# Performance work log

Measured on AMD Instinct MI355X. Metric: run time of the kernel, lower is better.

The kernel has to match this reference:

```python
import jax, jax.numpy as jnp
import numpy as np
import math

N_HEAD = 16
HEAD_DIM = 64  # n_embd // n_head = 1024 / 16
N_EMBD = 1024
B, T = 4, 4096
LIN_K = 1024


def setup_inputs() -> dict:
    key = jax.random.key(0)
    ks = jax.random.split(key, 7)
    s = 0.02
    return {
        "x": jax.random.normal(ks[0], (B, T, N_EMBD), dtype=jnp.float32),
        "W_attn": jax.random.normal(ks[1], (N_EMBD, 3 * N_EMBD), dtype=jnp.float32) * s,
        "b_attn": jax.random.normal(ks[2], (3 * N_EMBD,), dtype=jnp.float32) * s,
        "W_proj": jax.random.normal(ks[3], (N_EMBD, N_EMBD), dtype=jnp.float32) * s,
        "b_proj": jax.random.normal(ks[4], (N_EMBD,), dtype=jnp.float32) * s,
        "E": jax.random.normal(ks[5], (T, LIN_K), dtype=jnp.float32) * s,
        "F": jax.random.normal(ks[6], (T, LIN_K), dtype=jnp.float32) * s,
    }


def reference(x, W_attn, b_attn, W_proj, b_proj, E, F):
    Bb, Tt, C = x.shape
    qkv = x @ W_attn + b_attn                      # (B, T, 3C)
    q, k, v = jnp.split(qkv, 3, axis=-1)
    def heads(t):  # (B, T, C) -> (B, H, T, d)
        return t.reshape(Bb, Tt, N_HEAD, HEAD_DIM).transpose(0, 2, 1, 3)
    q, k, v = heads(q), heads(k), heads(v)
    # Linformer low-rank projection of K and V along the sequence axis
    k_proj = jnp.einsum('bhtd,tk->bhkd', k, E)     # (B, H, K, d)
    v_proj = jnp.einsum('bhtd,tk->bhkd', v, F)
    att = jnp.einsum('bhtd,bhkd->bhtk', q, k_proj) / math.sqrt(HEAD_DIM)
    # causal mask: position t may attend to projected slot j iff j <= t
    mask = jnp.arange(LIN_K)[None, :] <= jnp.arange(Tt)[:, None]  # (T, K)
    att = jnp.where(mask[None, None, :, :], att, -jnp.inf)
    att = jax.nn.softmax(att, axis=-1)
    y = jnp.einsum('bhtk,bhkd->bhtd', att, v_proj)
    y = y.transpose(0, 2, 1, 3).reshape(Bb, Tt, C)
    return y @ W_proj + b_proj
```

## Files before the change

### kernel.cpp

```cpp
#include <hip/hip_runtime.h>
#include <stdint.h>

typedef short bf16x8 __attribute__((ext_vector_type(8)));
typedef short bf16x4 __attribute__((ext_vector_type(4)));
typedef float f32x4 __attribute__((ext_vector_type(4)));
typedef float f32x16 __attribute__((ext_vector_type(16)));
typedef int i32x4 __attribute__((ext_vector_type(4)));

__device__ __forceinline__ short f2bf(float f) {
  union { float f; uint32_t u; } v; v.f = f;
  uint32_t r = (v.u + 0x7FFFu + ((v.u >> 16) & 1u)) >> 16;
  return (short)(uint16_t)r;
}

__device__ __forceinline__ int cvtpk(float lo, float hi) {
  int r;
  asm("v_cvt_pk_bf16_f32 %0, %1, %2" : "=v"(r) : "v"(lo), "v"(hi));
  return r;
}

__device__ __forceinline__ void gload16(const void* g, void* l) {
  __builtin_amdgcn_global_load_lds(
      (const __attribute__((address_space(1))) unsigned int*)g,
      (__attribute__((address_space(3))) unsigned int*)l, 16, 0, 0);
}

#define WAITV(n) asm volatile("s_waitcnt vmcnt(" #n ")" ::: "memory")
#define BARRIER()                          \
  do {                                     \
    __builtin_amdgcn_s_barrier();          \
    asm volatile("" ::: "memory");         \
  } while (0)

__global__ __launch_bounds__(256) void k_convert(const float* __restrict__ in,
                                                 short* __restrict__ out, int n) {
  int i = (blockIdx.x * 256 + threadIdx.x) * 4;
  if (i >= n) return;
  float4 v = *reinterpret_cast<const float4*>(in + i);
  bf16x4 o; o[0] = f2bf(v.x); o[1] = f2bf(v.y); o[2] = f2bf(v.z); o[3] = f2bf(v.w);
  *reinterpret_cast<bf16x4*>(out + i) = o;
}

__global__ __launch_bounds__(256) void k_transpose_cvt(const float* __restrict__ in,
                                                       short* __restrict__ out,
                                                       int R, int C) {
  __shared__ float tile[32][33];
  int r0 = blockIdx.y * 32, c0 = blockIdx.x * 32;
  int tx = threadIdx.x & 31, ty = threadIdx.x >> 5;
#pragma unroll
  for (int j = 0; j < 4; ++j)
    tile[ty + j * 8][tx] = in[(size_t)(r0 + ty + j * 8) * C + c0 + tx];
  __syncthreads();
#pragma unroll
  for (int j = 0; j < 4; ++j)
    out[(size_t)(c0 + ty + j * 8) * R + r0 + tx] = f2bf(tile[tx][ty + j * 8]);
}

__global__ __launch_bounds__(512, 2) void k_gemm_qkv(const short* __restrict__ A,
                                                     const short* __restrict__ BT,
                                                     const float* __restrict__ bias,
                                                     short* __restrict__ qb,
                                                     short* __restrict__ kT,
                                                     short* __restrict__ vT) {
  __shared__ __align__(16) char lds[4 * 32768];
  const int tid = threadIdx.x, l = tid & 63, wv = tid >> 6;
  const int wm = wv >> 2, wn = wv & 3;
  const int r16 = l & 15, g4 = l >> 4;
  const int orig = blockIdx.x;
  const int wg = (orig & 7) * 96 + (orig >> 3);
  const int m0 = (wg & 63) * 256, n0 = (wg >> 6) * 256;
  const int sl = (tid & 3) ^ ((tid >> 3) & 3);
  const short* aS = A + (size_t)(m0 + (tid >> 2)) * 1024 + sl * 8;
  const short* bS = BT + (size_t)(n0 + (tid >> 2)) * 1024 + sl * 8;
  const int sw = (g4 ^ ((r16 >> 1) & 3)) * 16;

  f32x4 acc[8][4];
#pragma unroll
  for (int i = 0; i < 8; ++i)
#pragma unroll
    for (int j = 0; j < 4; ++j) acc[i][j] = f32x4{0.f, 0.f, 0.f, 0.f};

#define STAGE1(kt, bf)                                                      \
  {                                                                         \
    const int k0_ = (kt) * 32;                                              \
    gload16(aS + k0_, lds + (bf) * 32768 + tid * 16);                       \
    gload16(aS + 131072 + k0_, lds + (bf) * 32768 + 8192 + tid * 16);       \
    gload16(bS + k0_, lds + (bf) * 32768 + 16384 + tid * 16);               \
    gload16(bS + 131072 + k0_, lds + (bf) * 32768 + 24576 + tid * 16);      \
  }

  STAGE1(0, 0); STAGE1(1, 1); STAGE1(2, 2);

  for (int kt = 0; kt < 32; ++kt) {
    if (kt < 30) WAITV(8);
    else if (kt == 30) WAITV(4);
    else WAITV(0);
    BARRIER();
    if (kt + 3 < 32) STAGE1(kt + 3, (kt + 3) & 3);
    const char* aT = lds + (kt & 3) * 32768;
    const char* bT = aT + 16384;
    bf16x8 af[8], bfr[4];
#pragma unroll
    for (int mi = 0; mi < 8; ++mi)
      af[mi] = *(const bf16x8*)(aT + (wm * 128 + mi * 16 + r16) * 64 + sw);
#pragma unroll
    for (int ni = 0; ni < 4; ++ni)
      bfr[ni] = *(const bf16x8*)(bT + (wn * 64 + ni * 16 + r16) * 64 + sw);
    __builtin_amdgcn_s_setprio(1);
#pragma unroll
    for (int mi = 0; mi < 8; ++mi)
#pragma unroll
      for (int ni = 0; ni < 4; ++ni)
        acc[mi][ni] = __builtin_amdgcn_mfma_f32_16x16x32_bf16(af[mi], bfr[ni], acc[mi][ni], 0, 0, 0);
    __builtin_amdgcn_s_setprio(0);
  }
#undef STAGE1

  const int seg = n0 >> 10;
#pragma unroll
  for (int i = 0; i < 8; ++i)
#pragma unroll
    for (int j = 0; j < 4; ++j) {
      int row = m0 + wm * 128 + i * 16 + g4 * 4;
      int colg = n0 + wn * 64 + j * 16 + r16;
      float bv = bias[colg];
      if (seg == 0) {
#pragma unroll
        for (int q = 0; q < 4; ++q)
          qb[(size_t)(row + q) * 1024 + colg] = f2bf(acc[i][j][q] + bv);
      } else {
        int c = colg & 1023;
        int bb = row >> 12, t = row & 4095;
        short* dst = (seg == 1) ? kT : vT;
        bf16x4 ov;
#pragma unroll
        for (int q = 0; q < 4; ++q) ov[q] = f2bf(acc[i][j][q] + bv);
        *reinterpret_cast<bf16x4*>(&dst[((size_t)(bb << 10) + c) * 4096 + t]) = ov;
      }
    }
}

__global__ __launch_bounds__(256, 2) void k_proj(const short* __restrict__ Et,
                                                 const short* __restrict__ Ft,
                                                 const short* __restrict__ kT,
                                                 const short* __restrict__ vT,
                                                 short* __restrict__ kp,
                                                 short* __restrict__ vpt) {
  const int z = blockIdx.z, b = z >> 1, which = z & 1;
  const short* __restrict__ AT = which ? Ft : Et;
  const short* __restrict__ BTp = (which ? vT : kT) + ((size_t)b << 10) * 4096;
  __shared__ __align__(16) char lds[4 * 16384];
  const int tid = threadIdx.x, l = tid & 63, wv = tid >> 6;
  const int wm = wv >> 1, wn = wv & 1;
  const int r16 = l & 15, g4 = l >> 4;
  const int m0 = blockIdx.x * 128, n0 = blockIdx.y * 128;
  const int sl = (tid & 3) ^ ((tid >> 3) & 3);
  const short* aS = AT + (size_t)(m0 + (tid >> 2)) * 4096 + sl * 8;
  const short* bS = BTp + (size_t)(n0 + (tid >> 2)) * 4096 + sl * 8;
  const int sw = (g4 ^ ((r16 >> 1) & 3)) * 16;

  f32x4 acc[4][4];
#pragma unroll
  for (int i = 0; i < 4; ++i)
#pragma unroll
    for (int j = 0; j < 4; ++j) acc[i][j] = f32x4{0.f, 0.f, 0.f, 0.f};

#define STAGE2(kt, bf)                                                      \
  {                                                                         \
    const int k0_ = (kt) * 32;                                              \
    gload16(aS + k0_, lds + (bf) * 16384 + tid * 16);                       \
    gload16(aS + 262144 + k0_, lds + (bf) * 16384 + 4096 + tid * 16);       \
    gload16(bS + k0_, lds + (bf) * 16384 + 8192 + tid * 16);                \
    gload16(bS + 262144 + k0_, lds + (bf) * 16384 + 12288 + tid * 16);      \
  }

  STAGE2(0, 0); STAGE2(1, 1); STAGE2(2, 2);

  for (int kt = 0; kt < 128; ++kt) {
    if (kt < 126) WAITV(8);
    else if (kt == 126) WAITV(4);
    else WAITV(0);
    BARRIER();
    if (kt + 3 < 128) STAGE2(kt + 3, (kt + 3) & 3);
    const char* aT = lds + (kt & 3) * 16384;
    const char* bT = aT + 8192;
    bf16x8 af[4], bfr[4];
#pragma unroll
    for (int mi = 0; mi < 4; ++mi)
      af[mi] = *(const bf16x8*)(aT + (wm * 64 + mi * 16 + r16) * 64 + sw);
#pragma unroll
    for (int ni = 0; ni < 4; ++ni)
      bfr[ni] = *(const bf16x8*)(bT + (wn * 64 + ni * 16 + r16) * 64 + sw);
    __builtin_amdgcn_s_setprio(1);
#pragma unroll
    for (int mi = 0; mi < 4; ++mi)
#pragma unroll
      for (int ni = 0; ni < 4; ++ni)
        acc[mi][ni] = __builtin_amdgcn_mfma_f32_16x16x32_bf16(af[mi], bfr[ni], acc[mi][ni], 0, 0, 0);
    __builtin_amdgcn_s_setprio(0);
  }
#undef STAGE2

  if (which) {
#pragma unroll
    for (int i = 0; i < 4; ++i)
#pragma unroll
      for (int j = 0; j < 4; ++j) {
        int row = m0 + wm * 64 + i * 16 + g4 * 4;
        int col = n0 + wn * 64 + j * 16 + r16;
        bf16x4 ov;
#pragma unroll
        for (int q = 0; q < 4; ++q) ov[q] = f2bf(acc[i][j][q]);
        *reinterpret_cast<bf16x4*>(&vpt[((size_t)(b * 1024) + col) * 1024 + row]) = ov;
      }
  } else {
#pragma unroll
    for (int i = 0; i < 4; ++i)
#pragma unroll
      for (int j = 0; j < 4; ++j) {
        int row = m0 + wm * 64 + i * 16 + g4 * 4;
        int col = n0 + wn * 64 + j * 16 + r16;
#pragma unroll
        for (int q = 0; q < 4; ++q)
          kp[((size_t)(b * 1024) + row + q) * 1024 + col] = f2bf(acc[i][j][q] * 0.125f);
      }
  }
}

__global__ __launch_bounds__(256, 3) void k_attn(const short* __restrict__ qb,
                                                 const short* __restrict__ kp,
                                                 const short* __restrict__ vpt,
                                                 short* __restrict__ y) {
  __shared__ __align__(16) char KsB[128 * 128];
  __shared__ __align__(16) char VtB[64 * 256];
  const int tid = threadIdx.x, lane = tid & 63, w = tid >> 6;
  const int r32 = lane & 31, hi = lane >> 5;
  const int iblk = 31 - blockIdx.x;
  const int bh = blockIdx.y, b = bh >> 4, h = bh & 15;
  const int t0 = iblk * 128;
  const int tl = w * 32 + r32;
  const int T = t0 + tl;

  bf16x8 qf[4];
#pragma unroll
  for (int kd = 0; kd < 4; ++kd)
    qf[kd] = *reinterpret_cast<const bf16x8*>(
        &qb[(size_t)(b * 4096 + T) * 1024 + h * 64 + kd * 16 + hi * 8]);

  f32x16 o[2];
#pragma unroll
  for (int i = 0; i < 16; ++i) { o[0][i] = 0.f; o[1][i] = 0.f; }
  float lrun = 0.f;

  const short* kpb = kp + ((size_t)b << 20) + h * 64;
  const short* vtb = vpt + (((size_t)b << 10) + h * 64) * 1024;

  const int kkl_ = tid >> 3, c8 = tid & 7;
  const int dl_ = tid >> 4, c16 = tid & 15;
  bf16x8 kreg[4], vreg[4];

#define LOADT(jt)                                                              \
  {                                                                            \
    const int kk0_ = (jt) * 128;                                               \
    _Pragma("unroll") for (int it = 0; it < 4; ++it) {                         \
      kreg[it] = *reinterpret_cast<const bf16x8*>(                             \
          &kpb[(size_t)(kk0_ + it * 32 + kkl_) * 1024 + c8 * 8]);              \
      vreg[it] = *reinterpret_cast<const bf16x8*>(                             \
          &vtb[(size_t)(it * 16 + dl_) * 1024 + kk0_ + c16 * 8]);              \
    }                                                                          \
  }

  LOADT(0);

  const int ntiles = (iblk + 1 < 8) ? (iblk + 1) : 8;
  for (int jt = 0; jt < ntiles; ++jt) {
    WAITV(0);
    BARRIER();
#pragma unroll
    for (int it = 0; it < 4; ++it) {
      int kk = it * 32 + kkl_;
      *reinterpret_cast<bf16x8*>(&KsB[kk * 128 + ((c8 * 16) ^ ((kk & 7) << 4))]) = kreg[it];
      int d = it * 16 + dl_;
      *reinterpret_cast<bf16x8*>(&VtB[d * 256 + ((c16 * 16) ^ ((d & 7) << 4))]) = vreg[it];
    }
    __syncthreads();
    if (jt + 1 < ntiles) LOADT(jt + 1);

#pragma unroll
    for (int st = 0; st < 2; ++st) {
      f32x16 s[2];
#pragma unroll
      for (int i = 0; i < 16; ++i) { s[0][i] = 0.f; s[1][i] = 0.f; }
#pragma unroll
      for (int ni = 0; ni < 2; ++ni) {
        int row = (st * 2 + ni) * 32 + r32;
#pragma unroll
        for (int kd = 0; kd < 4; ++kd) {
          bf16x8 kf = *reinterpret_cast<const bf16x8*>(
              &KsB[row * 128 + ((kd * 32 + hi * 16) ^ ((row & 7) << 4))]);
          s[ni] = __builtin_amdgcn_mfma_f32_32x32x16_bf16(kf, qf[kd], s[ni], 0, 0, 0);
        }
      }

      if (jt == iblk) {
#pragma unroll
        for (int ni = 0; ni < 2; ++ni)
#pragma unroll
          for (int j = 0; j < 16; ++j) {
            int kkl = (st * 2 + ni) * 32 + (j & 3) + 8 * (j >> 2) + 4 * hi;
            if (kkl > tl) s[ni][j] = -1e30f;
          }
      }

      float r0 = 0.f, r1 = 0.f, r2 = 0.f, r3 = 0.f;
#pragma unroll
      for (int j = 0; j < 16; j += 2) {
        float e0 = __expf(s[0][j]);
        float e1 = __expf(s[0][j + 1]);
        float e2 = __expf(s[1][j]);
        float e3 = __expf(s[1][j + 1]);
        s[0][j] = e0; s[0][j + 1] = e1; s[1][j] = e2; s[1][j + 1] = e3;
        r0 += e0; r1 += e1; r2 += e2; r3 += e3;
      }
      float rsum = (r0 + r1) + (r2 + r3);
      rsum += __shfl_xor(rsum, 32, 64);
      lrun += rsum;

#pragma unroll
      for (int kbl = 0; kbl < 4; ++kbl) {
        const int ni = kbl >> 1, jb = (kbl & 1) * 8;
        int lo0 = cvtpk(s[ni][jb + 0], s[ni][jb + 1]);
        int lo1 = cvtpk(s[ni][jb + 2], s[ni][jb + 3]);
        int hi0 = cvtpk(s[ni][jb + 4], s[ni][jb + 5]);
        int hi1 = cvtpk(s[ni][jb + 6], s[ni][jb + 7]);
        asm("v_permlane32_swap_b32 %0, %1" : "+v"(lo0), "+v"(hi0));
        asm("v_permlane32_swap_b32 %0, %1" : "+v"(lo1), "+v"(hi1));
        i32x4 pw; pw[0] = lo0; pw[1] = lo1; pw[2] = hi0; pw[3] = hi1;
        bf16x8 pf = __builtin_bit_cast(bf16x8, pw);
        const int kb = st * 4 + kbl;
#pragma unroll
        for (int mo = 0; mo < 2; ++mo) {
          int row = mo * 32 + r32;
          bf16x8 vf = *reinterpret_cast<const bf16x8*>(
              &VtB[row * 256 + ((kb * 32 + hi * 16) ^ ((row & 7) << 4))]);
          o[mo] = __builtin_amdgcn_mfma_f32_32x32x16_bf16(vf, pf, o[mo], 0, 0, 0);
        }
      }
    }
  }

  float inv = 1.0f / lrun;
#pragma unroll
  for (int mo = 0; mo < 2; ++mo)
#pragma unroll
    for (int rq = 0; rq < 4; ++rq) {
      bf16x4 ov;
#pragma unroll
      for (int c = 0; c < 4; ++c) ov[c] = f2bf(o[mo][rq * 4 + c] * inv);
      *reinterpret_cast<bf16x4*>(
          &y[(size_t)(b * 4096 + T) * 1024 + h * 64 + mo * 32 + rq * 8 + hi * 4]) = ov;
    }
#undef LOADT
}

__global__ __launch_bounds__(256, 2) void k_gemm_out(const short* __restrict__ A,
                                                     const short* __restrict__ BT,
                                                     const float* __restrict__ bias,
                                                     float* __restrict__ C) {
  __shared__ __align__(16) char lds[4 * 16384];
  const int tid = threadIdx.x, l = tid & 63, wv = tid >> 6;
  const int wm = wv >> 1, wn = wv & 1;
  const int r16 = l & 15, g4 = l >> 4;
  const int m0 = blockIdx.x * 128, n0 = blockIdx.y * 128;
  const int sl = (tid & 3) ^ ((tid >> 3) & 3);
  const short* aS = A + (size_t)(m0 + (tid >> 2)) * 1024 + sl * 8;
  const short* bS = BT + (size_t)(n0 + (tid >> 2)) * 1024 + sl * 8;
  const int sw = (g4 ^ ((r16 >> 1) & 3)) * 16;

  f32x4 acc[4][4];
#pragma unroll
  for (int i = 0; i < 4; ++i)
#pragma unroll
    for (int j = 0; j < 4; ++j) acc[i][j] = f32x4{0.f, 0.f, 0.f, 0.f};

#define STAGE3(kt, bf)                                                      \
  {                                                                         \
    const int k0_ = (kt) * 32;                                              \
    gload16(aS + k0_, lds + (bf) * 16384 + tid * 16);                       \
    gload16(aS + 65536 + k0_, lds + (bf) * 16384 + 4096 + tid * 16);        \
    gload16(bS + k0_, lds + (bf) * 16384 + 8192 + tid * 16);                \
    gload16(bS + 65536 + k0_, lds + (bf) * 16384 + 12288 + tid * 16);       \
  }

  STAGE3(0, 0); STAGE3(1, 1); STAGE3(2, 2);

  for (int kt = 0; kt < 32; ++kt) {
    if (kt < 30) WAITV(8);
    else if (kt == 30) WAITV(4);
    else WAITV(0);
    BARRIER();
    if (kt + 3 < 32) STAGE3(kt + 3, (kt + 3) & 3);
    const char* aT = lds + (kt & 3) * 16384;
    const char* bT = aT + 8192;
    bf16x8 af[4], bfr[4];
#pragma unroll
    for (int mi = 0; mi < 4; ++mi)
      af[mi] = *(const bf16x8*)(aT + (wm * 64 + mi * 16 + r16) * 64 + sw);
#pragma unroll
    for (int ni = 0; ni < 4; ++ni)
      bfr[ni] = *(const bf16x8*)(bT + (wn * 64 + ni * 16 + r16) * 64 + sw);
    __builtin_amdgcn_s_setprio(1);
#pragma unroll
    for (int mi = 0; mi < 4; ++mi)
#pragma unroll
      for (int ni = 0; ni < 4; ++ni)
        acc[mi][ni] = __builtin_amdgcn_mfma_f32_16x16x32_bf16(af[mi], bfr[ni], acc[mi][ni], 0, 0, 0);
    __builtin_amdgcn_s_setprio(0);
  }
#undef STAGE3

#pragma unroll
  for (int i = 0; i < 4; ++i)
#pragma unroll
    for (int j = 0; j < 4; ++j) {
      int row = m0 + wm * 64 + i * 16 + g4 * 4;
      int col = n0 + wn * 64 + j * 16 + r16;
      float bv = bias[col];
#pragma unroll
      for (int q = 0; q < 4; ++q)
        C[(size_t)(row + q) * 1024 + col] = acc[i][j][q] + bv;
    }
}

extern "C" void kernel_launch(void* const* d_in, const int* in_sizes, int n_in,
                              void* d_out, int out_size, void* d_ws, size_t ws_size,
                              hipStream_t stream) {
  const float* x      = (const float*)d_in[0];
  const float* W_attn = (const float*)d_in[1];
  const float* b_attn = (const float*)d_in[2];
  const float* W_proj = (const float*)d_in[3];
  const float* b_proj = (const float*)d_in[4];
  const float* E      = (const float*)d_in[5];
  const float* F      = (const float*)d_in[6];
  float* out = (float*)d_out;

  char* ws = (char*)d_ws;
  short* xb  = (short*)(ws + 0);
  short* WaT = (short*)(ws + 33554432);
  short* WpT = (short*)(ws + 39845888);
  short* Et  = (short*)(ws + 41943040);
  short* Ft  = (short*)(ws + 50331648);
  short* qb  = (short*)(ws + 58720256);
  short* kT  = (short*)(ws + 92274688);
  short* vT  = (short*)(ws + 125829120);
  short* kp  = (short*)(ws + 159383552);
  short* vpt = (short*)(ws + 167772160);
  short* yb  = (short*)(ws + 176160768);

  k_convert<<<16384, 256, 0, stream>>>(x, xb, 16777216);
  k_transpose_cvt<<<dim3(96, 32), 256, 0, stream>>>(W_attn, WaT, 1024, 3072);
  k_transpose_cvt<<<dim3(32, 32), 256, 0, stream>>>(W_proj, WpT, 1024, 1024);
  k_transpose_cvt<<<dim3(32, 128), 256, 0, stream>>>(E, Et, 4096, 1024);
  k_transpose_cvt<<<dim3(32, 128), 256, 0, stream>>>(F, Ft, 4096, 1024);

  k_gemm_qkv<<<768, 512, 0, stream>>>(xb, WaT, b_attn, qb, kT, vT);
  k_proj<<<dim3(8, 8, 8), 256, 0, stream>>>(Et, Ft, kT, vT, kp, vpt);
  k_attn<<<dim3(32, 64), 256, 0, stream>>>(qb, kp, vpt, yb);
  k_gemm_out<<<dim3(128, 8), 256, 0, stream>>>(yb, WpT, b_proj, out);
}
```

Measured before the change: 392.2 us.

## Interleave QKV GEMM global prefetch with MFMA phases and remap tiles per XCD

Splits each k-step of the QKV GEMM into four phases. Each phase loads two A fragments from LDS, issues one of the four global-to-LDS prefetch loads and runs eight MFMAs, with barriers between phases. The aim is to spread memory issue across compute instead of bursting it at the start of the step. It also changes the block-to-tile mapping so each XCD covers a contiguous group of eight M tiles, for better L2 reuse of A. The extra barriers per step add synchronisation cost and may stall waves.

```diff
diff --git a/kernel.cpp b/kernel.cpp
--- a/kernel.cpp
+++ b/kernel.cpp
@@ -67,8 +67,8 @@
   const int wm = wv >> 2, wn = wv & 3;
   const int r16 = l & 15, g4 = l >> 4;
   const int orig = blockIdx.x;
-  const int wg = (orig & 7) * 96 + (orig >> 3);
-  const int m0 = (wg & 63) * 256, n0 = (wg >> 6) * 256;
+  const int xcd = orig & 7, loc = orig >> 3;
+  const int m0 = (xcd * 8 + (loc & 7)) * 256, n0 = (loc >> 3) * 256;
   const int sl = (tid & 3) ^ ((tid >> 3) & 3);
   const short* aS = A + (size_t)(m0 + (tid >> 2)) * 1024 + sl * 8;
   const short* bS = BT + (size_t)(n0 + (tid >> 2)) * 1024 + sl * 8;
@@ -96,23 +96,39 @@
     else if (kt == 30) WAITV(4);
     else WAITV(0);
     BARRIER();
-    if (kt + 3 < 32) STAGE1(kt + 3, (kt + 3) & 3);
     const char* aT = lds + (kt & 3) * 32768;
     const char* bT = aT + 16384;
-    bf16x8 af[8], bfr[4];
-#pragma unroll
-    for (int mi = 0; mi < 8; ++mi)
-      af[mi] = *(const bf16x8*)(aT + (wm * 128 + mi * 16 + r16) * 64 + sw);
+    const int stg = (kt + 3 < 32);
+    char* dstB = lds + ((kt + 3) & 3) * 32768;
+    const int k0n = (kt + 3) * 32;
+
+    bf16x8 bfr[4];
 #pragma unroll
     for (int ni = 0; ni < 4; ++ni)
       bfr[ni] = *(const bf16x8*)(bT + (wn * 64 + ni * 16 + r16) * 64 + sw);
-    __builtin_amdgcn_s_setprio(1);
-#pragma unroll
-    for (int mi = 0; mi < 8; ++mi)
-#pragma unroll
-      for (int ni = 0; ni < 4; ++ni)
-        acc[mi][ni] = __builtin_amdgcn_mfma_f32_16x16x32_bf16(af[mi], bfr[ni], acc[mi][ni], 0, 0, 0);
-    __builtin_amdgcn_s_setprio(0);
+
+#pragma unroll
+    for (int ph = 0; ph < 4; ++ph) {
+      bf16x8 a0 = *(const bf16x8*)(aT + (wm * 128 + (2 * ph) * 16 + r16) * 64 + sw);
+      bf16x8 a1 = *(const bf16x8*)(aT + (wm * 128 + (2 * ph + 1) * 16 + r16) * 64 + sw);
+      if (stg) {
+        if (ph == 0)      gload16(aS + k0n, dstB + tid * 16);
+        else if (ph == 1) gload16(aS + 131072 + k0n, dstB + 8192 + tid * 16);
+        else if (ph == 2) gload16(bS + k0n, dstB + 16384 + tid * 16);
+        else              gload16(bS + 131072 + k0n, dstB + 24576 + tid * 16);
+      }
+      BARRIER();
+      __builtin_amdgcn_s_setprio(1);
+#pragma unroll
+      for (int ni = 0; ni < 4; ++ni) {
+        acc[2 * ph][ni] =
+            __builtin_amdgcn_mfma_f32_16x16x32_bf16(a0, bfr[ni], acc[2 * ph][ni], 0, 0, 0);
+        acc[2 * ph + 1][ni] =
+            __builtin_amdgcn_mfma_f32_16x16x32_bf16(a1, bfr[ni], acc[2 * ph + 1][ni], 0, 0, 0);
+      }
+      __builtin_amdgcn_s_setprio(0);
+      BARRIER();
+    }
   }
 #undef STAGE1
 
```

Measured after the change: 385.6 us. No clear change (-1.7%).

## Reassociate Linformer K/V projection to project x before weight GEMM

Applied to the files above, without the earlier changes.

Computes E^T x and F^T x directly from a transposed bf16 copy of x, then multiplies by the K/V weight slices and adds a bias term scaled by column sums of E/F. This removes the K and V parts of the large QKV GEMM over the full sequence, leaving only the Q GEMM. It adds transposes of x, a slow serial column-sum kernel, and a small extra GEMM, and rounding order changes slightly.

```diff
diff --git a/kernel.cpp b/kernel.cpp
--- a/kernel.cpp
+++ b/kernel.cpp
@@ -56,19 +56,29 @@
     out[(size_t)(c0 + ty + j * 8) * R + r0 + tx] = f2bf(tile[tx][ty + j * 8]);
 }
 
-__global__ __launch_bounds__(512, 2) void k_gemm_qkv(const short* __restrict__ A,
-                                                     const short* __restrict__ BT,
-                                                     const float* __restrict__ bias,
-                                                     short* __restrict__ qb,
-                                                     short* __restrict__ kT,
-                                                     short* __restrict__ vT) {
+__global__ __launch_bounds__(256) void k_colsum(const float* __restrict__ E,
+                                                const float* __restrict__ F,
+                                                float* __restrict__ sE,
+                                                float* __restrict__ sF) {
+  const int bid = blockIdx.x;
+  const int which = bid >> 2, c = (bid & 3) * 256 + threadIdx.x;
+  const float* src = which ? F : E;
+  float s = 0.f;
+  for (int t = 0; t < 4096; ++t) s += src[(size_t)t * 1024 + c];
+  (which ? sF : sE)[c] = s;
+}
+
+__global__ __launch_bounds__(512, 2) void k_gemm_q(const short* __restrict__ A,
+                                                   const short* __restrict__ BT,
+                                                   const float* __restrict__ bias,
+                                                   short* __restrict__ qb) {
   __shared__ __align__(16) char lds[4 * 32768];
   const int tid = threadIdx.x, l = tid & 63, wv = tid >> 6;
   const int wm = wv >> 2, wn = wv & 3;
   const int r16 = l & 15, g4 = l >> 4;
   const int orig = blockIdx.x;
-  const int wg = (orig & 7) * 96 + (orig >> 3);
-  const int m0 = (wg & 63) * 256, n0 = (wg >> 6) * 256;
+  const int xcd = orig & 7, loc = orig >> 3;
+  const int m0 = (xcd * 8 + (loc & 7)) * 256, n0 = (loc >> 3) * 256;
   const int sl = (tid & 3) ^ ((tid >> 3) & 3);
   const short* aS = A + (size_t)(m0 + (tid >> 2)) * 1024 + sl * 8;
   const short* bS = BT + (size_t)(n0 + (tid >> 2)) * 1024 + sl * 8;
@@ -80,7 +90,7 @@
 #pragma unroll
     for (int j = 0; j < 4; ++j) acc[i][j] = f32x4{0.f, 0.f, 0.f, 0.f};
 
-#define STAGE1(kt, bf)                                                      \
+#define STAGEQ(kt, bf)                                                      \
   {                                                                         \
     const int k0_ = (kt) * 32;                                              \
     gload16(aS + k0_, lds + (bf) * 32768 + tid * 16);                       \
@@ -89,14 +99,14 @@
     gload16(bS + 131072 + k0_, lds + (bf) * 32768 + 24576 + tid * 16);      \
   }
 
-  STAGE1(0, 0); STAGE1(1, 1); STAGE1(2, 2);
+  STAGEQ(0, 0); STAGEQ(1, 1); STAGEQ(2, 2);
 
   for (int kt = 0; kt < 32; ++kt) {
     if (kt < 30) WAITV(8);
     else if (kt == 30) WAITV(4);
     else WAITV(0);
     BARRIER();
-    if (kt + 3 < 32) STAGE1(kt + 3, (kt + 3) & 3);
+    if (kt + 3 < 32) STAGEQ(kt + 3, (kt + 3) & 3);
     const char* aT = lds + (kt & 3) * 32768;
     const char* bT = aT + 16384;
     bf16x8 af[8], bfr[4];
@@ -114,41 +124,30 @@
         acc[mi][ni] = __builtin_amdgcn_mfma_f32_16x16x32_bf16(af[mi], bfr[ni], acc[mi][ni], 0, 0, 0);
     __builtin_amdgcn_s_setprio(0);
   }
-#undef STAGE1
-
-  const int seg = n0 >> 10;
+#undef STAGEQ
+
 #pragma unroll
   for (int i = 0; i < 8; ++i)
 #pragma unroll
     for (int j = 0; j < 4; ++j) {
       int row = m0 + wm * 128 + i * 16 + g4 * 4;
-      int colg = n0 + wn * 64 + j * 16 + r16;
-      float bv = bias[colg];
-      if (seg == 0) {
-#pragma unroll
-        for (int q = 0; q < 4; ++q)
-          qb[(size_t)(row + q) * 1024 + colg] = f2bf(acc[i][j][q] + bv);
-      } else {
-        int c = colg & 1023;
-        int bb = row >> 12, t = row & 4095;
-        short* dst = (seg == 1) ? kT : vT;
-        bf16x4 ov;
-#pragma unroll
-        for (int q = 0; q < 4; ++q) ov[q] = f2bf(acc[i][j][q] + bv);
-        *reinterpret_cast<bf16x4*>(&dst[((size_t)(bb << 10) + c) * 4096 + t]) = ov;
-      }
+      int col = n0 + wn * 64 + j * 16 + r16;
+      float bv = bias[col];
+#pragma unroll
+      for (int q = 0; q < 4; ++q)
+        qb[(size_t)(row + q) * 1024 + col] = f2bf(acc[i][j][q] + bv);
     }
 }
 
 __global__ __launch_bounds__(256, 2) void k_proj(const short* __restrict__ Et,
                                                  const short* __restrict__ Ft,
-                                                 const short* __restrict__ kT,
-                                                 const short* __restrict__ vT,
-                                                 short* __restrict__ kp,
-                                                 short* __restrict__ vpt) {
+                                                 const short* __restrict__ xT,
+                                                 short* __restrict__ xEk,
+                                                 short* __restrict__ xEv) {
   const int z = blockIdx.z, b = z >> 1, which = z & 1;
   const short* __restrict__ AT = which ? Ft : Et;
-  const short* __restrict__ BTp = (which ? vT : kT) + ((size_t)b << 10) * 4096;
+  const short* __restrict__ BTp = xT + ((size_t)b << 10) * 4096;
+  short* __restrict__ outp = which ? xEv : xEk;
   __shared__ __align__(16) char lds[4 * 16384];
   const int tid = threadIdx.x, l = tid & 63, wv = tid >> 6;
   const int wm = wv >> 1, wn = wv & 1;
@@ -201,6 +200,83 @@
   }
 #undef STAGE2
 
+#pragma unroll
+  for (int i = 0; i < 4; ++i)
+#pragma unroll
+    for (int j = 0; j < 4; ++j) {
+      int row = m0 + wm * 64 + i * 16 + g4 * 4;
+      int col = n0 + wn * 64 + j * 16 + r16;
+#pragma unroll
+      for (int q = 0; q < 4; ++q)
+        outp[((size_t)(b * 1024) + row + q) * 1024 + col] = f2bf(acc[i][j][q]);
+    }
+}
+
+__global__ __launch_bounds__(256, 2) void k_kpvp(const short* __restrict__ xEk,
+                                                 const short* __restrict__ xEv,
+                                                 const short* __restrict__ WaT,
+                                                 const float* __restrict__ b_attn,
+                                                 const float* __restrict__ sE,
+                                                 const float* __restrict__ sF,
+                                                 short* __restrict__ kp,
+                                                 short* __restrict__ vpt) {
+  const int which = blockIdx.z;
+  const short* __restrict__ A = which ? xEv : xEk;
+  const short* __restrict__ BT = WaT + (size_t)(1024 + which * 1024) * 1024;
+  const float* __restrict__ bias = b_attn + 1024 + which * 1024;
+  const float* __restrict__ rs = which ? sF : sE;
+  __shared__ __align__(16) char lds[4 * 16384];
+  const int tid = threadIdx.x, l = tid & 63, wv = tid >> 6;
+  const int wm = wv >> 1, wn = wv & 1;
+  const int r16 = l & 15, g4 = l >> 4;
+  const int m0 = blockIdx.x * 128, n0 = blockIdx.y * 128;
+  const int sl = (tid & 3) ^ ((tid >> 3) & 3);
+  const short* aS = A + (size_t)(m0 + (tid >> 2)) * 1024 + sl * 8;
+  const short* bS = BT + (size_t)(n0 + (tid >> 2)) * 1024 + sl * 8;
+  const int sw = (g4 ^ ((r16 >> 1) & 3)) * 16;
+
+  f32x4 acc[4][4];
+#pragma unroll
+  for (int i = 0; i < 4; ++i)
+#pragma unroll
+    for (int j = 0; j < 4; ++j) acc[i][j] = f32x4{0.f, 0.f, 0.f, 0.f};
+
+#define STAGEP(kt, bf)                                                      \
+  {                                                                         \
+    const int k0_ = (kt) * 32;                                              \
+    gload16(aS + k0_, lds + (bf) * 16384 + tid * 16);                       \
+    gload16(aS + 65536 + k0_, lds + (bf) * 16384 + 4096 + tid * 16);        \
+    gload16(bS + k0_, lds + (bf) * 16384 + 8192 + tid * 16);                \
+    gload16(bS + 65536 + k0_, lds + (bf) * 16384 + 12288 + tid * 16);       \
+  }
+
+  STAGEP(0, 0); STAGEP(1, 1); STAGEP(2, 2);
+
+  for (int kt = 0; kt < 32; ++kt) {
+    if (kt < 30) WAITV(8);
+    else if (kt == 30) WAITV(4);
+    else WAITV(0);
+    BARRIER();
+    if (kt + 3 < 32) STAGEP(kt + 3, (kt + 3) & 3);
+    const char* aT = lds + (kt & 3) * 16384;
+    const char* bT = aT + 8192;
+    bf16x8 af[4], bfr[4];
+#pragma unroll
+    for (int mi = 0; mi < 4; ++mi)
+      af[mi] = *(const bf16x8*)(aT + (wm * 64 + mi * 16 + r16) * 64 + sw);
+#pragma unroll
+    for (int ni = 0; ni < 4; ++ni)
+      bfr[ni] = *(const bf16x8*)(bT + (wn * 64 + ni * 16 + r16) * 64 + sw);
+    __builtin_amdgcn_s_setprio(1);
+#pragma unroll
+    for (int mi = 0; mi < 4; ++mi)
+#pragma unroll
+      for (int ni = 0; ni < 4; ++ni)
+        acc[mi][ni] = __builtin_amdgcn_mfma_f32_16x16x32_bf16(af[mi], bfr[ni], acc[mi][ni], 0, 0, 0);
+    __builtin_amdgcn_s_setprio(0);
+  }
+#undef STAGEP
+
   if (which) {
 #pragma unroll
     for (int i = 0; i < 4; ++i)
@@ -208,10 +284,14 @@
       for (int j = 0; j < 4; ++j) {
         int row = m0 + wm * 64 + i * 16 + g4 * 4;
         int col = n0 + wn * 64 + j * 16 + r16;
+        int bb = row >> 10;
+        float bv = bias[col];
         bf16x4 ov;
 #pragma unroll
-        for (int q = 0; q < 4; ++q) ov[q] = f2bf(acc[i][j][q]);
-        *reinterpret_cast<bf16x4*>(&vpt[((size_t)(b * 1024) + col) * 1024 + row]) = ov;
+        for (int q = 0; q < 4; ++q)
+          ov[q] = f2bf(acc[i][j][q] + rs[(row + q) & 1023] * bv);
+        *reinterpret_cast<bf16x4*>(
+            &vpt[(((size_t)bb << 10) + col) * 1024 + (row & 1023)]) = ov;
       }
   } else {
 #pragma unroll
@@ -220,9 +300,11 @@
       for (int j = 0; j < 4; ++j) {
         int row = m0 + wm * 64 + i * 16 + g4 * 4;
         int col = n0 + wn * 64 + j * 16 + r16;
+        float bv = bias[col];
 #pragma unroll
         for (int q = 0; q < 4; ++q)
-          kp[((size_t)(b * 1024) + row + q) * 1024 + col] = f2bf(acc[i][j][q] * 0.125f);
+          kp[(size_t)(row + q) * 1024 + col] =
+              f2bf((acc[i][j][q] + rs[(row + q) & 1023] * bv) * 0.125f);
       }
   }
 }
@@ -451,20 +533,28 @@
   short* Et  = (short*)(ws + 41943040);
   short* Ft  = (short*)(ws + 50331648);
   short* qb  = (short*)(ws + 58720256);
-  short* kT  = (short*)(ws + 92274688);
-  short* vT  = (short*)(ws + 125829120);
-  short* kp  = (short*)(ws + 159383552);
-  short* vpt = (short*)(ws + 167772160);
-  short* yb  = (short*)(ws + 176160768);
+  short* xTb = (short*)(ws + 92274688);
+  short* xEk = (short*)(ws + 125829120);
+  short* xEv = (short*)(ws + 134217728);
+  short* kp  = (short*)(ws + 142606336);
+  short* vpt = (short*)(ws + 150994944);
+  short* yb  = (short*)(ws + 159383552);
+  float* sE  = (float*)(ws + 192937984);
+  float* sF  = (float*)(ws + 192942080);
 
   k_convert<<<16384, 256, 0, stream>>>(x, xb, 16777216);
   k_transpose_cvt<<<dim3(96, 32), 256, 0, stream>>>(W_attn, WaT, 1024, 3072);
   k_transpose_cvt<<<dim3(32, 32), 256, 0, stream>>>(W_proj, WpT, 1024, 1024);
   k_transpose_cvt<<<dim3(32, 128), 256, 0, stream>>>(E, Et, 4096, 1024);
   k_transpose_cvt<<<dim3(32, 128), 256, 0, stream>>>(F, Ft, 4096, 1024);
-
-  k_gemm_qkv<<<768, 512, 0, stream>>>(xb, WaT, b_attn, qb, kT, vT);
-  k_proj<<<dim3(8, 8, 8), 256, 0, stream>>>(Et, Ft, kT, vT, kp, vpt);
+  for (int b = 0; b < 4; ++b)
+    k_transpose_cvt<<<dim3(32, 128), 256, 0, stream>>>(
+        x + (size_t)b * 4096 * 1024, xTb + (size_t)b * 1024 * 4096, 4096, 1024);
+  k_colsum<<<8, 256, 0, stream>>>(E, F, sE, sF);
+
+  k_gemm_q<<<256, 512, 0, stream>>>(xb, WaT, b_attn, qb);
+  k_proj<<<dim3(8, 8, 8), 256, 0, stream>>>(Et, Ft, xTb, xEk, xEv);
+  k_kpvp<<<dim3(32, 8, 2), 256, 0, stream>>>(xEk, xEv, WaT, b_attn, sE, sF, kp, vpt);
   k_attn<<<dim3(32, 64), 256, 0, stream>>>(qb, kp, vpt, yb);
   k_gemm_out<<<dim3(128, 8), 256, 0, stream>>>(yb, WpT, b_proj, out);
 }
```

Measured after the change: 469.4 us. +19.7%, slower.
